# Performance work log

Hardware: AMD Instinct MI355X
Metric: run time of the kernel (lower is better)

Reference implementation:

```python
import jax, jax.numpy as jnp
import numpy as np

B, T, D_IN, EMB, H = 2, 2048, 1024, 1024, 16
HD = EMB // H  # head_dim = 64


def setup_inputs() -> dict:
    key = jax.random.key(0)
    ks = jax.random.split(key, 3)
    scale_qkv = 1.0 / np.sqrt(D_IN)
    scale_o = 1.0 / np.sqrt(EMB)
    return {
        "x": jax.random.normal(ks[0], (B, T, D_IN), dtype=jnp.float32),
        "W_qkv": jax.random.normal(ks[1], (D_IN, 3 * EMB), dtype=jnp.float32) * scale_qkv,
        "b_qkv": jnp.zeros((3 * EMB,), dtype=jnp.float32),
        "W_o": jax.random.normal(ks[2], (EMB, EMB), dtype=jnp.float32) * scale_o,
        "b_o": jnp.zeros((EMB,), dtype=jnp.float32),
    }


def reference(x, W_qkv, b_qkv, W_o, b_o):
    b, t, _ = x.shape
    qkv = x @ W_qkv + b_qkv                      # [B,T,3*EMB]
    # Match torch: reshape to (B,T,H,3*HD) -> permute -> chunk into q,k,v
    qkv = qkv.reshape(b, t, H, 3 * HD).transpose(0, 2, 1, 3)  # [B,H,T,3*HD]
    q, k, v = jnp.split(qkv, 3, axis=-1)         # each [B,H,T,HD]
    scale = 1.0 / jnp.sqrt(jnp.asarray(HD, dtype=q.dtype))
    scores = jnp.einsum("bhqd,bhkd->bhqk", q, k) * scale  # [B,H,T,T]
    attn = jax.nn.softmax(scores, axis=-1)
    values = jnp.einsum("bhqk,bhkd->bhqd", attn, v)       # [B,H,T,HD]
    values = values.transpose(0, 2, 1, 3).reshape(b, t, EMB)
    return values @ W_o + b_o
```

## Files before the change

kernel.cpp:

```cpp
#include <hip/hip_runtime.h>
#include <math.h>

typedef __bf16 bf16x8 __attribute__((ext_vector_type(8)));
typedef float f32x4 __attribute__((ext_vector_type(4)));

#define GPTR(p) ((const __attribute__((address_space(1))) void*)(p))
#define LPTR(p) ((__attribute__((address_space(3))) void*)(p))

#define QSCALE 0.18033688011112042f

__device__ __forceinline__ unsigned short f2bf(float f) {
  unsigned int u = __float_as_uint(f);
  u += 0x7FFFu + ((u >> 16) & 1u);
  return (unsigned short)(u >> 16);
}

__device__ __forceinline__ unsigned int pack_bf2(float lo, float hi) {
  return __builtin_amdgcn_perm(__float_as_uint(hi) + 0x8000u,
                               __float_as_uint(lo) + 0x8000u, 0x07060302u);
}

__device__ __forceinline__ float fast_exp2(float x) {
#if __has_builtin(__builtin_amdgcn_exp2f)
  return __builtin_amdgcn_exp2f(x);
#else
  return exp2f(x);
#endif
}

__device__ __forceinline__ f32x4 zero4() {
  f32x4 z; z[0] = 0.f; z[1] = 0.f; z[2] = 0.f; z[3] = 0.f; return z;
}

__device__ __forceinline__ void permlane_swap32(unsigned int& a, unsigned int& b) {
  asm("v_permlane32_swap_b32 %0, %1" : "+v"(a), "+v"(b));
}
__device__ __forceinline__ void permlane_swap16(unsigned int& a, unsigned int& b) {
  asm("v_permlane16_swap_b32 %0, %1" : "+v"(a), "+v"(b));
}

__global__ void conv_x_bf16(const float* __restrict__ in, unsigned short* __restrict__ out) {
  int i = (blockIdx.x * 256 + threadIdx.x) * 4;
  float4 v = *(const float4*)(in + i);
  ushort4 o;
  o.x = f2bf(v.x); o.y = f2bf(v.y); o.z = f2bf(v.z); o.w = f2bf(v.w);
  *(ushort4*)(out + i) = o;
}

__global__ void transpose_conv(const float* __restrict__ in, unsigned short* __restrict__ out,
                               int K, int N) {
  __shared__ float tile[64][65];
  int k0 = blockIdx.y * 64, n0 = blockIdx.x * 64;
  int t = threadIdx.x;
#pragma unroll
  for (int p = 0; p < 16; ++p) {
    int l = p * 256 + t; int r = l >> 6, c = l & 63;
    tile[r][c] = in[(size_t)(k0 + r) * N + n0 + c];
  }
  __syncthreads();
#pragma unroll
  for (int p = 0; p < 16; ++p) {
    int l = p * 256 + t; int r = l >> 6, c = l & 63;
    out[(size_t)(n0 + r) * K + k0 + c] = f2bf(tile[c][r]);
  }
}

__global__ __launch_bounds__(256) void gemm_qkv(
    const unsigned short* __restrict__ A, const unsigned short* __restrict__ Bt,
    const float* __restrict__ bias,
    unsigned short* __restrict__ Qd, unsigned short* __restrict__ Kd,
    unsigned short* __restrict__ Vtd) {
  __shared__ unsigned short As[2][4096];
  __shared__ unsigned short Bs[2][4096];
  const int tid = threadIdx.x, wave = tid >> 6, lane = tid & 63;
  const int quad = lane >> 4, l16 = lane & 15;
  const int wm = (wave >> 1) * 64, wn = (wave & 1) * 64;
  const int m0 = blockIdx.y * 128, n0 = blockIdx.x * 128;
  f32x4 acc[4][4];
#pragma unroll
  for (int i = 0; i < 4; ++i)
#pragma unroll
    for (int j = 0; j < 4; ++j) acc[i][j] = zero4();

  const int c = wave * 64 + lane;
  const int rA = c >> 2, o16 = (c & 3) * 8;

#define STAGEQ(B, K0)                                                                      \
  do {                                                                                     \
    __builtin_amdgcn_global_load_lds(GPTR(A + (size_t)(m0 + rA) * 1024 + (K0) + o16),      \
                                     LPTR(&As[B][wave * 512]), 16, 0, 0);                  \
    __builtin_amdgcn_global_load_lds(GPTR(A + (size_t)(m0 + 64 + rA) * 1024 + (K0) + o16), \
                                     LPTR(&As[B][2048 + wave * 512]), 16, 0, 0);           \
    __builtin_amdgcn_global_load_lds(GPTR(Bt + (size_t)(n0 + rA) * 1024 + (K0) + o16),     \
                                     LPTR(&Bs[B][wave * 512]), 16, 0, 0);                  \
    __builtin_amdgcn_global_load_lds(GPTR(Bt + (size_t)(n0 + 64 + rA) * 1024 + (K0) + o16),\
                                     LPTR(&Bs[B][2048 + wave * 512]), 16, 0, 0);           \
  } while (0)

  STAGEQ(0, 0);
  __syncthreads();
  int cur = 0;
  for (int k0 = 0; k0 < 1024; k0 += 32) {
    if (k0 < 992) STAGEQ(cur ^ 1, k0 + 32);
    bf16x8 af[4], bfr[4];
#pragma unroll
    for (int mt = 0; mt < 4; ++mt)
      af[mt] = *(const bf16x8*)(&As[cur][(wm + mt * 16 + l16) * 32 + quad * 8]);
#pragma unroll
    for (int nt = 0; nt < 4; ++nt)
      bfr[nt] = *(const bf16x8*)(&Bs[cur][(wn + nt * 16 + l16) * 32 + quad * 8]);
#pragma unroll
    for (int mt = 0; mt < 4; ++mt)
#pragma unroll
      for (int nt = 0; nt < 4; ++nt)
        acc[mt][nt] = __builtin_amdgcn_mfma_f32_16x16x32_bf16(af[mt], bfr[nt], acc[mt][nt], 0, 0, 0);
    __syncthreads();
    cur ^= 1;
  }
#undef STAGEQ

#pragma unroll
  for (int mt = 0; mt < 4; ++mt) {
#pragma unroll
    for (int nt = 0; nt < 4; ++nt) {
      int m = m0 + wm + mt * 16 + quad * 4;
      int n = n0 + wn + nt * 16 + l16;
      float bv = bias[n];
      int h = n / 192, rem = n - h * 192;
      int which = rem >> 6, d = rem & 63;
      int b = m >> 11, t0 = m & 2047;
      size_t head = (size_t)(b * 16 + h);
      f32x4 a = acc[mt][nt];
      if (which == 0) {
        size_t base = (head * 2048 + t0) * 64 + d;
#pragma unroll
        for (int i = 0; i < 4; ++i)
          Qd[base + (size_t)i * 64] = f2bf((a[i] + bv) * QSCALE);
      } else if (which == 1) {
        size_t base = head * 131072 + (size_t)(t0 >> 6) * 4096;
#pragma unroll
        for (int i = 0; i < 4; ++i) {
          int tt = t0 + i;
          Kd[base + (tt & 63) * 64 + (((d >> 3) ^ (tt & 7)) << 3) + (d & 7)] = f2bf(a[i] + bv);
        }
      } else {
        size_t base = head * 131072 + (size_t)(t0 >> 6) * 4096;
        ushort4 o;
        o.x = f2bf(a[0] + bv); o.y = f2bf(a[1] + bv);
        o.z = f2bf(a[2] + bv); o.w = f2bf(a[3] + bv);
        *(ushort4*)(Vtd + base + d * 64 + (((((t0 & 63) >> 3)) ^ (d & 7)) << 3) + (t0 & 7)) = o;
      }
    }
  }
}

__global__ __launch_bounds__(256) void flash_attn(
    const unsigned short* __restrict__ Qg,
    const unsigned short* __restrict__ Kg,
    const unsigned short* __restrict__ Vg,
    unsigned short* __restrict__ att) {
  __shared__ unsigned short Ks[2][4096];
  __shared__ unsigned short Vs[2][4096];
  const int tid = threadIdx.x, wave = tid >> 6, lane = tid & 63;
  const int quad = lane >> 4, l16 = lane & 15;
  const int h7 = l16 & 7;
  const int bh = blockIdx.y;
  const int q0 = blockIdx.x * 128 + wave * 32;

  bf16x8 bq[2][2];
#pragma unroll
  for (int qg = 0; qg < 2; ++qg)
#pragma unroll
    for (int kh = 0; kh < 2; ++kh)
      bq[qg][kh] = *(const bf16x8*)(Qg + ((size_t)bh * 2048 + q0 + qg * 16 + l16) * 64 + kh * 32 + quad * 8);

  f32x4 o[2][4];
#pragma unroll
  for (int qg = 0; qg < 2; ++qg)
#pragma unroll
    for (int i = 0; i < 4; ++i) o[qg][i] = zero4();
  float l_run[2] = {0.f, 0.f};

  const unsigned short* Kt = Kg + (size_t)bh * 131072 + lane * 8;
  const unsigned short* Vt = Vg + (size_t)bh * 131072 + lane * 8;
  const int so0 = wave * 512, so1 = (4 + wave) * 512;

#define STAGE_KV(buf, tile)                                                              \
  do {                                                                                   \
    const unsigned short* Kb_ = Kt + (tile) * 4096;                                      \
    const unsigned short* Vb_ = Vt + (tile) * 4096;                                      \
    __builtin_amdgcn_global_load_lds(GPTR(Kb_ + so0), LPTR(&Ks[buf][so0]), 16, 0, 0);    \
    __builtin_amdgcn_global_load_lds(GPTR(Kb_ + so1), LPTR(&Ks[buf][so1]), 16, 0, 0);    \
    __builtin_amdgcn_global_load_lds(GPTR(Vb_ + so0), LPTR(&Vs[buf][so0]), 16, 0, 0);    \
    __builtin_amdgcn_global_load_lds(GPTR(Vb_ + so1), LPTR(&Vs[buf][so1]), 16, 0, 0);    \
  } while (0)

  STAGE_KV(0, 0);
  __syncthreads();

  int cur = 0;
  for (int tile = 0; tile < 32; ++tile) {
    if (tile < 31) STAGE_KV(cur ^ 1, tile + 1);

    f32x4 s[2][4];
#pragma unroll
    for (int qg = 0; qg < 2; ++qg)
#pragma unroll
      for (int kt = 0; kt < 4; ++kt) s[qg][kt] = zero4();
#pragma unroll
    for (int kt = 0; kt < 4; ++kt) {
#pragma unroll
      for (int kh = 0; kh < 2; ++kh) {
        bf16x8 a = *(const bf16x8*)(&Ks[cur][(kt * 16 + l16) * 64 + (((kh * 4 + quad) ^ h7) << 3)]);
        s[0][kt] = __builtin_amdgcn_mfma_f32_16x16x32_bf16(a, bq[0][kh], s[0][kt], 0, 0, 0);
        s[1][kt] = __builtin_amdgcn_mfma_f32_16x16x32_bf16(a, bq[1][kh], s[1][kt], 0, 0, 0);
      }
    }

    unsigned int pw[2][4][2];
#pragma unroll
    for (int qg = 0; qg < 2; ++qg) {
      float lsum = 0.f;
      float pv[4][4];
#pragma unroll
      for (int kt = 0; kt < 4; ++kt)
#pragma unroll
        for (int r = 0; r < 4; ++r) {
          float p = fast_exp2(s[qg][kt][r]);
          pv[kt][r] = p;
          lsum += p;
        }
#pragma unroll
      for (int kt = 0; kt < 4; ++kt) {
        pw[qg][kt][0] = pack_bf2(pv[kt][0], pv[kt][1]);
        pw[qg][kt][1] = pack_bf2(pv[kt][2], pv[kt][3]);
      }
      lsum += __shfl_xor(lsum, 16);
      lsum += __shfl_xor(lsum, 32);
      l_run[qg] += lsum;
    }

    bf16x8 pf[2][2];
#pragma unroll
    for (int qg = 0; qg < 2; ++qg) {
#pragma unroll
      for (int st = 0; st < 2; ++st) {
        unsigned int a0 = pw[qg][2 * st][0], b0 = pw[qg][2 * st + 1][0];
        unsigned int a1 = pw[qg][2 * st][1], b1 = pw[qg][2 * st + 1][1];
        permlane_swap32(a0, b0); permlane_swap16(a0, b0);
        permlane_swap32(a1, b1); permlane_swap16(a1, b1);
        union { unsigned int u[4]; bf16x8 v; } x;
        x.u[0] = a0; x.u[1] = a1; x.u[2] = b0; x.u[3] = b1;
        pf[qg][st] = x.v;
      }
    }

#pragma unroll
    for (int st = 0; st < 2; ++st) {
#pragma unroll
      for (int mt = 0; mt < 4; ++mt) {
        bf16x8 av = *(const bf16x8*)(&Vs[cur][(mt * 16 + l16) * 64 + (((st * 4 + quad) ^ h7) << 3)]);
        o[0][mt] = __builtin_amdgcn_mfma_f32_16x16x32_bf16(av, pf[0][st], o[0][mt], 0, 0, 0);
        o[1][mt] = __builtin_amdgcn_mfma_f32_16x16x32_bf16(av, pf[1][st], o[1][mt], 0, 0, 0);
      }
    }

    __syncthreads();
    cur ^= 1;
  }
#undef STAGE_KV

  int b = bh >> 4, h = bh & 15;
#pragma unroll
  for (int qg = 0; qg < 2; ++qg) {
    float inv_l = 1.f / l_run[qg];
    unsigned short* orow = att + ((size_t)b * 2048 + q0 + qg * 16 + l16) * 1024 + h * 64;
#pragma unroll
    for (int mt = 0; mt < 4; ++mt) {
      ushort4 ov;
      ov.x = f2bf(o[qg][mt][0] * inv_l);
      ov.y = f2bf(o[qg][mt][1] * inv_l);
      ov.z = f2bf(o[qg][mt][2] * inv_l);
      ov.w = f2bf(o[qg][mt][3] * inv_l);
      *(ushort4*)(orow + mt * 16 + quad * 4) = ov;
    }
  }
}

__global__ __launch_bounds__(256) void gemm_out(
    const unsigned short* __restrict__ A, const unsigned short* __restrict__ Bt,
    const float* __restrict__ bias, float* __restrict__ out) {
  __shared__ unsigned short As[2][4096];
  __shared__ unsigned short Bs[2][2048];
  const int tid = threadIdx.x, wave = tid >> 6, lane = tid & 63;
  const int quad = lane >> 4, l16 = lane & 15;
  const int wm = (wave >> 1) * 64, wn = (wave & 1) * 32;
  const int m0 = blockIdx.y * 128, n0 = blockIdx.x * 64;
  f32x4 acc[4][2];
#pragma unroll
  for (int i = 0; i < 4; ++i)
#pragma unroll
    for (int j = 0; j < 2; ++j) acc[i][j] = zero4();

  const int c = wave * 64 + lane;
  const int rA = c >> 2, o16 = (c & 3) * 8;

#define STAGEO(B, K0)                                                                      \
  do {                                                                                     \
    __builtin_amdgcn_global_load_lds(GPTR(A + (size_t)(m0 + rA) * 1024 + (K0) + o16),      \
                                     LPTR(&As[B][wave * 512]), 16, 0, 0);                  \
    __builtin_amdgcn_global_load_lds(GPTR(A + (size_t)(m0 + 64 + rA) * 1024 + (K0) + o16), \
                                     LPTR(&As[B][2048 + wave * 512]), 16, 0, 0);           \
    __builtin_amdgcn_global_load_lds(GPTR(Bt + (size_t)(n0 + rA) * 1024 + (K0) + o16),     \
                                     LPTR(&Bs[B][wave * 512]), 16, 0, 0);                  \
  } while (0)

  STAGEO(0, 0);
  __syncthreads();
  int cur = 0;
  for (int k0 = 0; k0 < 1024; k0 += 32) {
    if (k0 < 992) STAGEO(cur ^ 1, k0 + 32);
    bf16x8 af[4], bfr[2];
#pragma unroll
    for (int mt = 0; mt < 4; ++mt)
      af[mt] = *(const bf16x8*)(&As[cur][(wm + mt * 16 + l16) * 32 + quad * 8]);
#pragma unroll
    for (int nt = 0; nt < 2; ++nt)
      bfr[nt] = *(const bf16x8*)(&Bs[cur][(wn + nt * 16 + l16) * 32 + quad * 8]);
#pragma unroll
    for (int mt = 0; mt < 4; ++mt)
#pragma unroll
      for (int nt = 0; nt < 2; ++nt)
        acc[mt][nt] = __builtin_amdgcn_mfma_f32_16x16x32_bf16(af[mt], bfr[nt], acc[mt][nt], 0, 0, 0);
    __syncthreads();
    cur ^= 1;
  }
#undef STAGEO

#pragma unroll
  for (int mt = 0; mt < 4; ++mt) {
#pragma unroll
    for (int nt = 0; nt < 2; ++nt) {
      int m = m0 + wm + mt * 16 + quad * 4;
      int n = n0 + wn + nt * 16 + l16;
      float bv = bias[n];
      float* orow = out + (size_t)m * 1024 + n;
      orow[0]        = acc[mt][nt][0] + bv;
      orow[1024]     = acc[mt][nt][1] + bv;
      orow[2 * 1024] = acc[mt][nt][2] + bv;
      orow[3 * 1024] = acc[mt][nt][3] + bv;
    }
  }
}

extern "C" void kernel_launch(void* const* d_in, const int* in_sizes, int n_in,
                              void* d_out, int out_size, void* d_ws, size_t ws_size,
                              hipStream_t stream) {
  const float* x    = (const float*)d_in[0];
  const float* Wqkv = (const float*)d_in[1];
  const float* bqkv = (const float*)d_in[2];
  const float* Wo   = (const float*)d_in[3];
  const float* bo   = (const float*)d_in[4];
  float* out = (float*)d_out;

  unsigned short* xb    = (unsigned short*)d_ws;
  unsigned short* wqkvt = xb    + (size_t)4096 * 1024;
  unsigned short* wot   = wqkvt + (size_t)3072 * 1024;
  unsigned short* Qd    = wot   + (size_t)1024 * 1024;
  unsigned short* Kd    = Qd    + (size_t)32 * 2048 * 64;
  unsigned short* Vtd   = Kd    + (size_t)32 * 2048 * 64;
  unsigned short* attb  = Vtd   + (size_t)32 * 2048 * 64;

  conv_x_bf16<<<4096, 256, 0, stream>>>(x, xb);
  transpose_conv<<<dim3(48, 16), 256, 0, stream>>>(Wqkv, wqkvt, 1024, 3072);
  transpose_conv<<<dim3(16, 16), 256, 0, stream>>>(Wo, wot, 1024, 1024);
  gemm_qkv<<<dim3(24, 32), 256, 0, stream>>>(xb, wqkvt, bqkv, Qd, Kd, Vtd);
  flash_attn<<<dim3(16, 32), 256, 0, stream>>>(Qd, Kd, Vtd, attb);
  gemm_out<<<dim3(16, 32), 256, 0, stream>>>(attb, wot, bo, out);
}
```

Before: 204.3 us.

## Split flash attention waves across key halves with LDS reduction of partial outputs

Each wave now covers 64 queries and half of each 64-key tile, instead of 32 queries over the whole tile. Each K/V fragment read from LDS is therefore reused across four query groups, and the per-tile row-sum shuffles move out of the loop into a single final reduction. Partial outputs and row sums from the two key-half waves are combined through shared memory before normalization. This raises accumulator register pressure (launch_bounds now requests 2 blocks) and adds an end-of-kernel LDS reduction and barrier.

Result: faster. 198.8 us (-2.7%).

```diff
diff --git a/kernel.cpp b/kernel.cpp
--- a/kernel.cpp
+++ b/kernel.cpp
@@ -154,45 +154,48 @@
   }
 }
 
-__global__ __launch_bounds__(256) void flash_attn(
+__global__ __launch_bounds__(256, 2) void flash_attn(
     const unsigned short* __restrict__ Qg,
     const unsigned short* __restrict__ Kg,
     const unsigned short* __restrict__ Vg,
     unsigned short* __restrict__ att) {
-  __shared__ unsigned short Ks[2][4096];
-  __shared__ unsigned short Vs[2][4096];
+  __shared__ unsigned short SM[16384];
+  __shared__ float Lbuf[2][64];
   const int tid = threadIdx.x, wave = tid >> 6, lane = tid & 63;
   const int quad = lane >> 4, l16 = lane & 15;
   const int h7 = l16 & 7;
+  const int wq = wave >> 1, wk = wave & 1;
   const int bh = blockIdx.y;
-  const int q0 = blockIdx.x * 128 + wave * 32;
-
-  bf16x8 bq[2][2];
-#pragma unroll
-  for (int qg = 0; qg < 2; ++qg)
+  const int q0 = blockIdx.x * 128 + wq * 64;
+
+  bf16x8 bq[4][2];
+#pragma unroll
+  for (int qg = 0; qg < 4; ++qg)
 #pragma unroll
     for (int kh = 0; kh < 2; ++kh)
       bq[qg][kh] = *(const bf16x8*)(Qg + ((size_t)bh * 2048 + q0 + qg * 16 + l16) * 64 + kh * 32 + quad * 8);
 
-  f32x4 o[2][4];
-#pragma unroll
-  for (int qg = 0; qg < 2; ++qg)
+  f32x4 o[4][4];
+#pragma unroll
+  for (int qg = 0; qg < 4; ++qg)
 #pragma unroll
     for (int i = 0; i < 4; ++i) o[qg][i] = zero4();
-  float l_run[2] = {0.f, 0.f};
+  float l_run[4] = {0.f, 0.f, 0.f, 0.f};
 
   const unsigned short* Kt = Kg + (size_t)bh * 131072 + lane * 8;
   const unsigned short* Vt = Vg + (size_t)bh * 131072 + lane * 8;
+  unsigned short* KsB = SM;
+  unsigned short* VsB = SM + 8192;
   const int so0 = wave * 512, so1 = (4 + wave) * 512;
 
 #define STAGE_KV(buf, tile)                                                              \
   do {                                                                                   \
     const unsigned short* Kb_ = Kt + (tile) * 4096;                                      \
     const unsigned short* Vb_ = Vt + (tile) * 4096;                                      \
-    __builtin_amdgcn_global_load_lds(GPTR(Kb_ + so0), LPTR(&Ks[buf][so0]), 16, 0, 0);    \
-    __builtin_amdgcn_global_load_lds(GPTR(Kb_ + so1), LPTR(&Ks[buf][so1]), 16, 0, 0);    \
-    __builtin_amdgcn_global_load_lds(GPTR(Vb_ + so0), LPTR(&Vs[buf][so0]), 16, 0, 0);    \
-    __builtin_amdgcn_global_load_lds(GPTR(Vb_ + so1), LPTR(&Vs[buf][so1]), 16, 0, 0);    \
+    __builtin_amdgcn_global_load_lds(GPTR(Kb_ + so0), LPTR(KsB + (buf) * 4096 + so0), 16, 0, 0); \
+    __builtin_amdgcn_global_load_lds(GPTR(Kb_ + so1), LPTR(KsB + (buf) * 4096 + so1), 16, 0, 0); \
+    __builtin_amdgcn_global_load_lds(GPTR(Vb_ + so0), LPTR(VsB + (buf) * 4096 + so0), 16, 0, 0); \
+    __builtin_amdgcn_global_load_lds(GPTR(Vb_ + so1), LPTR(VsB + (buf) * 4096 + so1), 16, 0, 0); \
   } while (0)
 
   STAGE_KV(0, 0);
@@ -201,29 +204,30 @@
   int cur = 0;
   for (int tile = 0; tile < 32; ++tile) {
     if (tile < 31) STAGE_KV(cur ^ 1, tile + 1);
-
-    f32x4 s[2][4];
-#pragma unroll
-    for (int qg = 0; qg < 2; ++qg)
-#pragma unroll
-      for (int kt = 0; kt < 4; ++kt) s[qg][kt] = zero4();
-#pragma unroll
-    for (int kt = 0; kt < 4; ++kt) {
+    const unsigned short* Kc = KsB + cur * 4096;
+    const unsigned short* Vc = VsB + cur * 4096;
+
+    f32x4 s[4][2];
+#pragma unroll
+    for (int qg = 0; qg < 4; ++qg) { s[qg][0] = zero4(); s[qg][1] = zero4(); }
+#pragma unroll
+    for (int kt = 0; kt < 2; ++kt) {
 #pragma unroll
       for (int kh = 0; kh < 2; ++kh) {
-        bf16x8 a = *(const bf16x8*)(&Ks[cur][(kt * 16 + l16) * 64 + (((kh * 4 + quad) ^ h7) << 3)]);
-        s[0][kt] = __builtin_amdgcn_mfma_f32_16x16x32_bf16(a, bq[0][kh], s[0][kt], 0, 0, 0);
-        s[1][kt] = __builtin_amdgcn_mfma_f32_16x16x32_bf16(a, bq[1][kh], s[1][kt], 0, 0, 0);
+        bf16x8 a = *(const bf16x8*)(Kc + (wk * 32 + kt * 16 + l16) * 64 + (((kh * 4 + quad) ^ h7) << 3));
+#pragma unroll
+        for (int qg = 0; qg < 4; ++qg)
+          s[qg][kt] = __builtin_amdgcn_mfma_f32_16x16x32_bf16(a, bq[qg][kh], s[qg][kt], 0, 0, 0);
       }
     }
 
-    unsigned int pw[2][4][2];
-#pragma unroll
-    for (int qg = 0; qg < 2; ++qg) {
+    unsigned int pw[4][2][2];
+#pragma unroll
+    for (int qg = 0; qg < 4; ++qg) {
       float lsum = 0.f;
-      float pv[4][4];
-#pragma unroll
-      for (int kt = 0; kt < 4; ++kt)
+      float pv[2][4];
+#pragma unroll
+      for (int kt = 0; kt < 2; ++kt)
 #pragma unroll
         for (int r = 0; r < 4; ++r) {
           float p = fast_exp2(s[qg][kt][r]);
@@ -231,38 +235,31 @@
           lsum += p;
         }
 #pragma unroll
-      for (int kt = 0; kt < 4; ++kt) {
+      for (int kt = 0; kt < 2; ++kt) {
         pw[qg][kt][0] = pack_bf2(pv[kt][0], pv[kt][1]);
         pw[qg][kt][1] = pack_bf2(pv[kt][2], pv[kt][3]);
       }
-      lsum += __shfl_xor(lsum, 16);
-      lsum += __shfl_xor(lsum, 32);
       l_run[qg] += lsum;
     }
 
-    bf16x8 pf[2][2];
-#pragma unroll
-    for (int qg = 0; qg < 2; ++qg) {
-#pragma unroll
-      for (int st = 0; st < 2; ++st) {
-        unsigned int a0 = pw[qg][2 * st][0], b0 = pw[qg][2 * st + 1][0];
-        unsigned int a1 = pw[qg][2 * st][1], b1 = pw[qg][2 * st + 1][1];
-        permlane_swap32(a0, b0); permlane_swap16(a0, b0);
-        permlane_swap32(a1, b1); permlane_swap16(a1, b1);
-        union { unsigned int u[4]; bf16x8 v; } x;
-        x.u[0] = a0; x.u[1] = a1; x.u[2] = b0; x.u[3] = b1;
-        pf[qg][st] = x.v;
-      }
-    }
-
-#pragma unroll
-    for (int st = 0; st < 2; ++st) {
-#pragma unroll
-      for (int mt = 0; mt < 4; ++mt) {
-        bf16x8 av = *(const bf16x8*)(&Vs[cur][(mt * 16 + l16) * 64 + (((st * 4 + quad) ^ h7) << 3)]);
-        o[0][mt] = __builtin_amdgcn_mfma_f32_16x16x32_bf16(av, pf[0][st], o[0][mt], 0, 0, 0);
-        o[1][mt] = __builtin_amdgcn_mfma_f32_16x16x32_bf16(av, pf[1][st], o[1][mt], 0, 0, 0);
-      }
+    bf16x8 pf[4];
+#pragma unroll
+    for (int qg = 0; qg < 4; ++qg) {
+      unsigned int a0 = pw[qg][0][0], b0 = pw[qg][1][0];
+      unsigned int a1 = pw[qg][0][1], b1 = pw[qg][1][1];
+      permlane_swap32(a0, b0); permlane_swap16(a0, b0);
+      permlane_swap32(a1, b1); permlane_swap16(a1, b1);
+      union { unsigned int u[4]; bf16x8 v; } x;
+      x.u[0] = a0; x.u[1] = a1; x.u[2] = b0; x.u[3] = b1;
+      pf[qg] = x.v;
+    }
+
+#pragma unroll
+    for (int mt = 0; mt < 4; ++mt) {
+      bf16x8 av = *(const bf16x8*)(Vc + (mt * 16 + l16) * 64 + (((wk * 4 + quad) ^ h7) << 3));
+#pragma unroll
+      for (int qg = 0; qg < 4; ++qg)
+        o[qg][mt] = __builtin_amdgcn_mfma_f32_16x16x32_bf16(av, pf[qg], o[qg][mt], 0, 0, 0);
     }
 
     __syncthreads();
@@ -270,19 +267,42 @@
   }
 #undef STAGE_KV
 
-  int b = bh >> 4, h = bh & 15;
-#pragma unroll
-  for (int qg = 0; qg < 2; ++qg) {
-    float inv_l = 1.f / l_run[qg];
-    unsigned short* orow = att + ((size_t)b * 2048 + q0 + qg * 16 + l16) * 1024 + h * 64;
-#pragma unroll
-    for (int mt = 0; mt < 4; ++mt) {
-      ushort4 ov;
-      ov.x = f2bf(o[qg][mt][0] * inv_l);
-      ov.y = f2bf(o[qg][mt][1] * inv_l);
-      ov.z = f2bf(o[qg][mt][2] * inv_l);
-      ov.w = f2bf(o[qg][mt][3] * inv_l);
-      *(ushort4*)(orow + mt * 16 + quad * 4) = ov;
+#pragma unroll
+  for (int qg = 0; qg < 4; ++qg) {
+    l_run[qg] += __shfl_xor(l_run[qg], 16);
+    l_run[qg] += __shfl_xor(l_run[qg], 32);
+  }
+
+  float* Obuf = (float*)SM;
+  if (wk == 1) {
+#pragma unroll
+    for (int qg = 0; qg < 4; ++qg) {
+#pragma unroll
+      for (int mt = 0; mt < 4; ++mt) {
+        int cc = (mt * 4 + quad) ^ l16;
+        *(f32x4*)(Obuf + wq * 4096 + (qg * 16 + l16) * 64 + cc * 4) = o[qg][mt];
+      }
+      if (quad == 0) Lbuf[wq][qg * 16 + l16] = l_run[qg];
+    }
+  }
+  __syncthreads();
+  if (wk == 0) {
+    int b = bh >> 4, h = bh & 15;
+#pragma unroll
+    for (int qg = 0; qg < 4; ++qg) {
+      float inv_l = 1.f / (l_run[qg] + Lbuf[wq][qg * 16 + l16]);
+      unsigned short* orow = att + ((size_t)b * 2048 + q0 + qg * 16 + l16) * 1024 + h * 64;
+#pragma unroll
+      for (int mt = 0; mt < 4; ++mt) {
+        int cc = (mt * 4 + quad) ^ l16;
+        f32x4 other = *(const f32x4*)(Obuf + wq * 4096 + (qg * 16 + l16) * 64 + cc * 4);
+        ushort4 ov;
+        ov.x = f2bf((o[qg][mt][0] + other[0]) * inv_l);
+        ov.y = f2bf((o[qg][mt][1] + other[1]) * inv_l);
+        ov.z = f2bf((o[qg][mt][2] + other[2]) * inv_l);
+        ov.w = f2bf((o[qg][mt][3] + other[3]) * inv_l);
+        *(ushort4*)(orow + mt * 16 + quad * 4) = ov;
+      }
     }
   }
 }
```
